# Kernel tuning notes

Measured on AMD Instinct MI355X. Metric: run time of the kernel, lower is better.

## Reference

```python
import jax, jax.numpy as jnp
import numpy as np

B, N, D = 8, 1024, 768
R, SH = 10, 2
H = R + SH            # 12 total heads
DH = D // H           # 64
DF = 2 * D            # FFN hidden


def _layernorm(x, g, b, eps=1e-5):
    mu = jnp.mean(x, axis=-1, keepdims=True)
    var = jnp.var(x, axis=-1, keepdims=True)
    return (x - mu) * jax.lax.rsqrt(var + eps) * g + b


def setup_inputs() -> dict:
    key = jax.random.key(0)
    ks = jax.random.split(key, 12)
    s = 0.02
    inp = {
        'nodes': jax.random.normal(ks[0], (B, N, D), dtype=jnp.float32),
        'relation_mask': jax.random.uniform(ks[1], (B, N, N, R), dtype=jnp.float32),
        'node_mask': jax.random.randint(ks[2], (B, N), 0, 2).astype(bool),
        'Wq': jax.random.normal(ks[3], (D, D), dtype=jnp.float32) * s,
        'bq': jnp.zeros((D,), jnp.float32),
        'Wk': jax.random.normal(ks[4], (D, D), dtype=jnp.float32) * s,
        'bk': jnp.zeros((D,), jnp.float32),
        'Wv': jax.random.normal(ks[5], (D, D), dtype=jnp.float32) * s,
        'bv': jnp.zeros((D,), jnp.float32),
        'Wo': jax.random.normal(ks[6], (D, D), dtype=jnp.float32) * s,
        'bo': jnp.zeros((D,), jnp.float32),
        'ln1_g': jnp.ones((D,), jnp.float32),
        'ln1_b': jnp.zeros((D,), jnp.float32),
        'W1': jax.random.normal(ks[7], (DF, D), dtype=jnp.float32) * s,
        'b1': jnp.zeros((DF,), jnp.float32),
        'W2': jax.random.normal(ks[8], (D, DF), dtype=jnp.float32) * s,
        'b2': jnp.zeros((D,), jnp.float32),
        'ln2_g': jnp.ones((D,), jnp.float32),
        'ln2_b': jnp.zeros((D,), jnp.float32),
    }
    return inp


def reference(nodes, relation_mask, node_mask, Wq, bq, Wk, bk, Wv, bv, Wo, bo,
              ln1_g, ln1_b, W1, b1, W2, b2, ln2_g, ln2_b):
    neg_inf = jnp.float32(-jnp.inf)
    # projections -> [B, H, N, DH]
    q = (nodes @ Wq.T + bq).reshape(B, N, H, DH).transpose(0, 2, 1, 3)
    k = (nodes @ Wk.T + bk).reshape(B, N, H, DH).transpose(0, 2, 1, 3)
    v = (nodes @ Wv.T + bv).reshape(B, N, H, DH).transpose(0, 2, 1, 3)
    scores = jnp.einsum('bhqd,bhkd->bhqk', q, k) / jnp.sqrt(jnp.float32(DH))
    # relation-typed gating on first R heads
    rel_gate = relation_mask.transpose(0, 3, 1, 2)          # [B, R, N, N]
    typed = jnp.where(rel_gate < 1e-4, neg_inf, scores[:, :R])
    scores = jnp.concatenate([typed, scores[:, R:]], axis=1)
    # key padding mask
    key_mask = node_mask[:, None, None, :]                  # [B,1,1,N]
    scores = jnp.where(key_mask, scores, neg_inf)
    attn = jax.nn.softmax(scores, axis=-1)
    attn = jnp.nan_to_num(attn, nan=0.0)                    # rows with no valid keys -> 0
    out = jnp.einsum('bhqk,bhkd->bhqd', attn, v)
    out = out.transpose(0, 2, 1, 3).reshape(B, N, D)
    out = out @ Wo.T + bo
    h = _layernorm(nodes + out, ln1_g, ln1_b)
    ffn = jax.nn.gelu(h @ W1.T + b1, approximate=False) @ W2.T + b2
    h = _layernorm(h + ffn, ln2_g, ln2_b)
    return h
```

## Files before the change

### kernel.cpp

```cpp
#include <hip/hip_runtime.h>
#include <stdint.h>
#include <math.h>

typedef unsigned short u16;
typedef __bf16 bf16x8 __attribute__((ext_vector_type(8)));
typedef __bf16 bf16x2 __attribute__((ext_vector_type(2)));
typedef unsigned short u16x8 __attribute__((ext_vector_type(8)));
typedef float f32x4 __attribute__((ext_vector_type(4)));

#define DEVI __device__ __forceinline__

constexpr int B_ = 8, N_ = 1024, D_ = 768, H_ = 12, DH_ = 64, DF_ = 1536;

DEVI u16 f2bu(float f) {
  unsigned x = __builtin_bit_cast(unsigned, f);
  x += 0x7FFFu + ((x >> 16) & 1u);
  return (u16)(x >> 16);
}
DEVI float b2f(u16 u) { return __builtin_bit_cast(float, (unsigned)u << 16); }

DEVI bf16x8 ld_frag(const u16* p) {
  return __builtin_bit_cast(bf16x8, *(const u16x8*)p);
}

DEVI void gload_lds16(const u16* g, u16* l) {
  __builtin_amdgcn_global_load_lds(
      (const __attribute__((address_space(1))) void*)g,
      (__attribute__((address_space(3))) void*)l, 16, 0, 0);
}

struct CvtArgs {
  const float* src[7];
  u16* dst[7];
  int n4[7];
  int start[8];
};
__global__ __launch_bounds__(256)
void prep_all(CvtArgs a, const float* __restrict__ rel, const int* __restrict__ nm,
              u16* __restrict__ mp) {
  const int gb0 = blockIdx.x;
  const int t = threadIdx.x;
  if (gb0 < 2048) {
    const int b = gb0 >> 8, q0 = ((gb0 >> 2) & 63) * 16, k0 = (gb0 & 3) * 256;
    __shared__ u16 w12[16][256];
    const int key_ok = nm[(b << 10) + k0 + t];
    const float th = 1e-4f;
#pragma unroll 1
    for (int it = 0; it < 16; ++it) {
      unsigned bits;
      if (!key_ok) {
        bits = 0xFFFu;
      } else {
        const size_t idx = (((size_t)(b << 10) + q0 + it) << 10) + k0 + t;
        const float2* rp = (const float2*)(rel + idx * 10);
        float2 a0 = rp[0], a1 = rp[1], a2 = rp[2], a3 = rp[3], a4 = rp[4];
        bits  = (a0.x < th ? 1u : 0u)   | (a0.y < th ? 2u : 0u)
              | (a1.x < th ? 4u : 0u)   | (a1.y < th ? 8u : 0u)
              | (a2.x < th ? 16u : 0u)  | (a2.y < th ? 32u : 0u)
              | (a3.x < th ? 64u : 0u)  | (a3.y < th ? 128u : 0u)
              | (a4.x < th ? 256u : 0u) | (a4.y < th ? 512u : 0u);
      }
      w12[it][t ^ ((it & 7) << 1)] = (u16)bits;
    }
    __syncthreads();
    const int ql = t & 15, kt = t >> 4;
    unsigned wv[16];
#pragma unroll
    for (int j2 = 0; j2 < 8; ++j2) {
      const int e = (kt * 16 + j2 * 2) ^ ((ql & 7) << 1);
      wv[j2 * 2] = w12[ql][e];
      wv[j2 * 2 + 1] = w12[ql][e + 1];
    }
#pragma unroll
    for (int h = 0; h < 12; ++h) {
      unsigned word = 0;
#pragma unroll
      for (int j = 0; j < 16; ++j) word |= ((wv[j] >> h) & 1u) << j;
      mp[(((size_t)(b * H_ + h)) * (N_ / 16) + (k0 >> 4) + kt) * N_ + q0 + ql] = (u16)word;
    }
  } else {
    int j = 0;
    while (gb0 >= a.start[j + 1]) ++j;
    const int i = (gb0 - a.start[j]) * 256 + t;
    if (i >= a.n4[j]) return;
    float4 v = ((const float4*)a.src[j])[i];
    ushort4 o;
    o.x = f2bu(v.x); o.y = f2bu(v.y); o.z = f2bu(v.z); o.w = f2bu(v.w);
    ((ushort4*)a.dst[j])[i] = o;
  }
}

template<int EPI>
DEVI void gemm_body(const u16* __restrict__ A, const u16* __restrict__ Bm,
                    const float* __restrict__ bias0, const float* __restrict__ bias1,
                    const float* __restrict__ residf, const u16* __restrict__ residb,
                    u16* __restrict__ out0, u16* __restrict__ out1,
                    int N, int K, int bx, int by,
                    u16 (&As)[3][128 * 32], u16 (&Bs)[3][128 * 32]) {
  const int t = threadIdx.x;
  const int w = t >> 6, l = t & 63;
  const int li = l & 15, grp = l >> 4;
  const int n0 = bx * 128, m0 = by * 128;
  const int wr = w >> 1, wc = w & 1;

  f32x4 acc[4][4] = {};

  const int arow = w * 16 + (l >> 2);
  const int acol = (l & 3) * 8;
  const u16* Ag = A + (size_t)(m0 + arow) * K + acol;
  const u16* Bg = Bm + (size_t)(n0 + arow) * K + acol;
  const int NT = K >> 5;

  auto stage = [&](int buf, int kt) {
    u16* Asw = &As[buf][(w * 16) * 32];
    u16* Bsw = &Bs[buf][(w * 16) * 32];
    const int k0 = kt * 32;
    gload_lds16(Ag + k0, Asw);
    gload_lds16(Ag + (size_t)64 * K + k0, Asw + 64 * 32);
    gload_lds16(Bg + k0, Bsw);
    gload_lds16(Bg + (size_t)64 * K + k0, Bsw + 64 * 32);
  };

  stage(0, 0); stage(1, 1);
  asm volatile("s_waitcnt vmcnt(4)\n\ts_barrier" ::: "memory");

  for (int kt = 0; kt < NT; ++kt) {
    const int bt = kt % 3;
    const bool pre = (kt + 2 < NT);
    if (pre) stage((kt + 2) % 3, kt + 2);
    bf16x8 af[4], bfr[4];
#pragma unroll
    for (int m = 0; m < 4; ++m)
      af[m] = ld_frag(&As[bt][(wr * 64 + m * 16 + li) * 32 + grp * 8]);
#pragma unroll
    for (int n = 0; n < 4; ++n)
      bfr[n] = ld_frag(&Bs[bt][(wc * 64 + n * 16 + li) * 32 + grp * 8]);
    __builtin_amdgcn_s_setprio(1);
#pragma unroll
    for (int m = 0; m < 4; ++m)
#pragma unroll
      for (int n = 0; n < 4; ++n)
        acc[m][n] = __builtin_amdgcn_mfma_f32_16x16x32_bf16(af[m], bfr[n], acc[m][n], 0, 0, 0);
    __builtin_amdgcn_s_setprio(0);
    if (pre) asm volatile("s_waitcnt vmcnt(4) lgkmcnt(0)\n\ts_barrier" ::: "memory");
    else     asm volatile("s_waitcnt vmcnt(0) lgkmcnt(0)\n\ts_barrier" ::: "memory");
  }

#pragma unroll
  for (int m = 0; m < 4; ++m) {
#pragma unroll
    for (int n = 0; n < 4; ++n) {
#pragma unroll
      for (int j = 0; j < 4; ++j) {
        const int row = m0 + wr * 64 + m * 16 + grp * 4 + j;
        const int col = n0 + wc * 64 + n * 16 + li;
        float v = acc[m][n][j];
        if constexpr (EPI == 0) {
          v += (col < D_) ? bias0[col] : bias1[col - D_];
          if (col < D_) v *= 0.125f;
          const int b = row >> 10, i = row & (N_ - 1);
          int c2 = (col < D_) ? col : col - D_;
          u16* dst = (col < D_) ? out0 : out1;
          dst[(((size_t)(b * H_ + (c2 >> 6))) * N_ + i) * DH_ + (c2 & 63)] = f2bu(v);
        } else if constexpr (EPI == 1) {
          v += bias0[row];
          const int b = col >> 10, i = col & (N_ - 1);
          out0[(((size_t)(b * H_ + (row >> 6))) * DH_ + (row & 63)) * N_ + i] = f2bu(v);
        } else if constexpr (EPI == 2) {
          v += bias0[col] + residf[(size_t)row * N + col];
          out0[(size_t)row * N + col] = f2bu(v);
        } else if constexpr (EPI == 3) {
          v += bias0[col];
          float gel = 0.5f * v * (1.0f + erff(v * 0.70710678118654752440f));
          out0[(size_t)row * N + col] = f2bu(gel);
        } else {
          v += bias0[col] + b2f(residb[(size_t)row * N + col]);
          out0[(size_t)row * N + col] = f2bu(v);
        }
      }
    }
  }
}

template<int EPI>
__global__ __launch_bounds__(256, 3)
void gemm_bt(const u16* __restrict__ A, const u16* __restrict__ Bm,
             const float* __restrict__ bias0,
             const float* __restrict__ residf, const u16* __restrict__ residb,
             u16* __restrict__ out0, int N, int K) {
  __shared__ u16 As[3][128 * 32];
  __shared__ u16 Bs[3][128 * 32];
  const int nwg = gridDim.x * gridDim.y;
  int id = blockIdx.y * gridDim.x + blockIdx.x;
  id = (id & 7) * (nwg >> 3) + (id >> 3);
  const int by = id / gridDim.x;
  const int bx = id - by * gridDim.x;
  gemm_body<EPI>(A, Bm, bias0, nullptr, residf, residb, out0, nullptr,
                 N, K, bx, by, As, Bs);
}

__global__ __launch_bounds__(256, 3)
void gemm_qkv(const u16* __restrict__ Xbf, const u16* __restrict__ Wqk,
              const u16* __restrict__ Wv,
              const float* __restrict__ bq, const float* __restrict__ bk,
              const float* __restrict__ bv,
              u16* __restrict__ qb, u16* __restrict__ kb, u16* __restrict__ vTb) {
  __shared__ u16 As[3][128 * 32];
  __shared__ u16 Bs[3][128 * 32];
  constexpr int nwg = 1152;
  int id = blockIdx.x;
  id = (id & 7) * (nwg >> 3) + (id >> 3);
  if (id < 768) {
    const int by = id / 12, bx = id - by * 12;
    gemm_body<0>(Xbf, Wqk, bq, bk, nullptr, nullptr, qb, kb,
                 1536, 768, bx, by, As, Bs);
  } else {
    const int v = id - 768;
    const int by = v / 64, bx = v - by * 64;
    gemm_body<1>(Wv, Xbf, bv, nullptr, nullptr, nullptr, vTb, nullptr,
                 8192, 768, bx, by, As, Bs);
  }
}

__global__ __launch_bounds__(512, 4)
void attn(const u16* __restrict__ q, const u16* __restrict__ k, const u16* __restrict__ vT,
          const u16* __restrict__ mp, u16* __restrict__ outp) {
  const int nwg = gridDim.x;
  const int p = blockIdx.x;
  const int lid = (p & 7) * (nwg >> 3) + (p >> 3);
  const int bh_i = lid >> 3;
  const int qblk = lid & 7;
  const int b = bh_i / H_, h = bh_i - (bh_i / H_) * H_;
  const int w = threadIdx.x >> 6, l = threadIdx.x & 63;
  const int li = l & 15, grp = l >> 4;
  const int qw = qblk * 128 + w * 16;
  const size_t bh = (size_t)bh_i;

  __shared__ u16 Kt[2][64 * 64];
  __shared__ u16 Vt[2][64 * 64];
  __shared__ u16 P[8][16 * 64];

  const u16* kbase = k + bh * N_ * DH_;
  const u16* vbase = vT + bh * DH_ * N_;

  const int srow_off = l >> 3;
  const int sg = l & 7;
  const int r0 = w * 8;
  auto stageK = [&](int buf, int kj0) {
    const int row = r0 + srow_off;
    const int gp = sg ^ (row & 7);
    gload_lds16(kbase + (size_t)(kj0 + row) * DH_ + gp * 8, &Kt[buf][r0 * 64]);
  };
  auto stageV = [&](int buf, int kj0) {
    const int row = r0 + srow_off;
    const int gp = sg ^ (row & 7);
    gload_lds16(vbase + (size_t)row * N_ + kj0 + gp * 8, &Vt[buf][r0 * 64]);
  };

  const u16* qp = q + (bh * N_ + qw) * DH_;
  const bf16x8 bq0 = ld_frag(qp + li * DH_ + grp * 8);
  const bf16x8 bq1 = ld_frag(qp + li * DH_ + 32 + grp * 8);

  f32x4 accO[4] = {};
  float m = -INFINITY, lsum = 0.f;

  u16* Pw = &P[w][0];
  const int sw = (li & 7) << 3;
  const int prow = li * 64;
  const u16* mrow = mp + bh * (N_ / 16) * N_ + qw + li;

  stageK(0, 0); stageV(0, 0);
  __syncthreads();
  int cur = 0;

  for (int kj0 = 0; kj0 < N_; kj0 += 64) {
    if (kj0 + 64 < N_) { stageK(cur ^ 1, kj0 + 64); stageV(cur ^ 1, kj0 + 64); }
    unsigned mword[4];
#pragma unroll
    for (int t = 0; t < 4; ++t) mword[t] = mrow[(size_t)((kj0 >> 4) + t) * N_];

    f32x4 s[4];
    __builtin_amdgcn_s_setprio(1);
#pragma unroll
    for (int t = 0; t < 4; ++t) {
      const int row = t * 16 + li;
      const int rs = row & 7;
      const bf16x8 ka0 = ld_frag(&Kt[cur][row * 64 + ((grp ^ rs) * 8)]);
      const bf16x8 ka1 = ld_frag(&Kt[cur][row * 64 + (((grp + 4) ^ rs) * 8)]);
      f32x4 z = {0.f, 0.f, 0.f, 0.f};
      z = __builtin_amdgcn_mfma_f32_16x16x32_bf16(ka0, bq0, z, 0, 0, 0);
      z = __builtin_amdgcn_mfma_f32_16x16x32_bf16(ka1, bq1, z, 0, 0, 0);
      s[t] = z;
    }
    __builtin_amdgcn_s_setprio(0);

    float sv[16];
#pragma unroll
    for (int t = 0; t < 4; ++t) {
      const unsigned mb = (mword[t] >> (grp * 4)) & 0xFu;
#pragma unroll
      for (int j = 0; j < 4; ++j)
        sv[t * 4 + j] = ((mb >> j) & 1u) ? -INFINITY : s[t][j];
    }
    const float a0 = fmaxf(fmaxf(sv[0], sv[1]), sv[2]);
    const float a1 = fmaxf(fmaxf(sv[3], sv[4]), sv[5]);
    const float a2 = fmaxf(fmaxf(sv[6], sv[7]), sv[8]);
    const float a3 = fmaxf(fmaxf(sv[9], sv[10]), sv[11]);
    const float a4 = fmaxf(fmaxf(sv[12], sv[13]), sv[14]);
    float rmax = fmaxf(fmaxf(fmaxf(a0, a1), fmaxf(a2, a3)), fmaxf(a4, sv[15]));
    rmax = fmaxf(rmax, __shfl_xor(rmax, 16));
    rmax = fmaxf(rmax, __shfl_xor(rmax, 32));
    if (!__all(rmax <= m + 8.f)) {
      const float mnew = fmaxf(m, rmax);
      const float scal = (m == -INFINITY) ? 0.f : __expf(m - mnew);
      lsum *= scal;
#pragma unroll
      for (int t2 = 0; t2 < 4; ++t2) accO[t2] *= scal;
      m = mnew;
    }
    const float msafe = (m == -INFINITY) ? 0.f : m;
    float psum = 0.f;
    float pv[16];
#pragma unroll
    for (int i = 0; i < 16; ++i) {
      const float e = __expf(sv[i] - msafe);
      pv[i] = e;
      psum += e;
    }
    psum += __shfl_xor(psum, 16);
    psum += __shfl_xor(psum, 32);
    lsum += psum;
#pragma unroll
    for (int t = 0; t < 4; ++t) {
      bf16x2 plo = { (__bf16)pv[t * 4 + 0], (__bf16)pv[t * 4 + 1] };
      bf16x2 phi = { (__bf16)pv[t * 4 + 2], (__bf16)pv[t * 4 + 3] };
      uint2 pk;
      pk.x = __builtin_bit_cast(unsigned, plo);
      pk.y = __builtin_bit_cast(unsigned, phi);
      *(uint2*)&Pw[prow + ((t * 16 + grp * 4) ^ sw)] = pk;
    }
    __builtin_amdgcn_s_setprio(1);
#pragma unroll
    for (int kc = 0; kc < 2; ++kc) {
      const bf16x8 pb = ld_frag(&Pw[prow + ((kc * 32 + grp * 8) ^ sw)]);
#pragma unroll
      for (int t2 = 0; t2 < 4; ++t2) {
        const int row = t2 * 16 + li;
        const bf16x8 va = ld_frag(&Vt[cur][row * 64 + (((kc * 4 + grp) ^ (row & 7)) * 8)]);
        accO[t2] = __builtin_amdgcn_mfma_f32_16x16x32_bf16(va, pb, accO[t2], 0, 0, 0);
      }
    }
    __builtin_amdgcn_s_setprio(0);
    __syncthreads();
    cur ^= 1;
  }
  const float inv = (lsum > 0.f) ? 1.0f / lsum : 0.f;
  u16* op = outp + ((size_t)b * N_ + qw + li) * D_ + h * DH_;
#pragma unroll
  for (int t2 = 0; t2 < 4; ++t2) {
    bf16x2 o01 = { (__bf16)(accO[t2][0] * inv), (__bf16)(accO[t2][1] * inv) };
    bf16x2 o23 = { (__bf16)(accO[t2][2] * inv), (__bf16)(accO[t2][3] * inv) };
    uint2 ov;
    ov.x = __builtin_bit_cast(unsigned, o01);
    ov.y = __builtin_bit_cast(unsigned, o23);
    *(uint2*)&op[t2 * 16 + grp * 4] = ov;
  }
}

template<int OUTF32>
__global__ __launch_bounds__(256)
void ln_kernel(const u16* __restrict__ x, const float* __restrict__ g,
               const float* __restrict__ be, u16* __restrict__ ybf,
               float* __restrict__ yf) {
  const int row = blockIdx.x;
  const int t = threadIdx.x;
  const u16* xr = x + (size_t)row * D_;
  const float v0 = b2f(xr[t]), v1 = b2f(xr[t + 256]), v2 = b2f(xr[t + 512]);
  float s = v0 + v1 + v2;
  float s2 = v0 * v0 + v1 * v1 + v2 * v2;
#pragma unroll
  for (int d = 1; d < 64; d <<= 1) { s += __shfl_xor(s, d); s2 += __shfl_xor(s2, d); }
  __shared__ float red[8];
  const int w = t >> 6;
  if ((t & 63) == 0) { red[w] = s; red[4 + w] = s2; }
  __syncthreads();
  s = red[0] + red[1] + red[2] + red[3];
  s2 = red[4] + red[5] + red[6] + red[7];
  const float mu = s * (1.0f / D_);
  const float var = fmaxf(s2 * (1.0f / D_) - mu * mu, 0.0f);
  const float rstd = rsqrtf(var + 1e-5f);
#pragma unroll
  for (int c = 0; c < 3; ++c) {
    const int idx = t + c * 256;
    const float vv = (c == 0) ? v0 : (c == 1) ? v1 : v2;
    const float o = (vv - mu) * rstd * g[idx] + be[idx];
    if constexpr (OUTF32) yf[(size_t)row * D_ + idx] = o;
    else ybf[(size_t)row * D_ + idx] = f2bu(o);
  }
}

extern "C" void kernel_launch(void* const* d_in, const int* in_sizes, int n_in,
                              void* d_out, int out_size, void* d_ws, size_t ws_size,
                              hipStream_t stream) {
  (void)in_sizes; (void)n_in; (void)out_size; (void)ws_size;
  const float* nodes = (const float*)d_in[0];
  const float* rel   = (const float*)d_in[1];
  const int*   nmask = (const int*)d_in[2];
  const float* Wq = (const float*)d_in[3];
  const float* bq = (const float*)d_in[4];
  const float* Wk = (const float*)d_in[5];
  const float* bk = (const float*)d_in[6];
  const float* Wv = (const float*)d_in[7];
  const float* bv = (const float*)d_in[8];
  const float* Wo = (const float*)d_in[9];
  const float* bo = (const float*)d_in[10];
  const float* ln1g = (const float*)d_in[11];
  const float* ln1b = (const float*)d_in[12];
  const float* W1 = (const float*)d_in[13];
  const float* b1 = (const float*)d_in[14];
  const float* W2 = (const float*)d_in[15];
  const float* b2 = (const float*)d_in[16];
  const float* ln2g = (const float*)d_in[17];
  const float* ln2b = (const float*)d_in[18];
  float* out = (float*)d_out;

  char* ws = (char*)d_ws;
  u16* Wqk_bf = (u16*)(ws + 0);
  u16* Wv_bf  = (u16*)(ws + 2359296);
  u16* Wo_bf  = (u16*)(ws + 3538944);
  u16* W1_bf  = (u16*)(ws + 4718592);
  u16* W2_bf  = (u16*)(ws + 7077888);
  u16* Xbf    = (u16*)(ws + 9437184);
  u16* qb     = (u16*)(ws + 22020096);
  u16* kb     = (u16*)(ws + 34603008);
  u16* vTb    = (u16*)(ws + 47185920);
  u16* mwb    = (u16*)(ws + 59768832);
  u16* prehb  = (u16*)(ws + 22020096);
  u16* hbf    = (u16*)(ws + 47185920);
  u16* f1b    = (u16*)(ws + 59768832);
  u16* preob  = (u16*)(ws + 84934656);
  u16* attno  = Xbf;

  const dim3 blk(256);
  CvtArgs ca;
  ca.src[0] = Wq; ca.src[1] = Wk; ca.src[2] = Wv; ca.src[3] = Wo;
  ca.src[4] = W1; ca.src[5] = W2; ca.src[6] = nodes;
  ca.dst[0] = Wqk_bf; ca.dst[1] = Wqk_bf + 768 * 768; ca.dst[2] = Wv_bf;
  ca.dst[3] = Wo_bf; ca.dst[4] = W1_bf; ca.dst[5] = W2_bf; ca.dst[6] = Xbf;
  ca.n4[0] = ca.n4[1] = ca.n4[2] = ca.n4[3] = 147456;
  ca.n4[4] = ca.n4[5] = 294912; ca.n4[6] = 1572864;
  ca.start[0] = 2048; ca.start[1] = 2624; ca.start[2] = 3200; ca.start[3] = 3776;
  ca.start[4] = 4352; ca.start[5] = 5504; ca.start[6] = 6656; ca.start[7] = 12800;
  prep_all<<<12800, blk, 0, stream>>>(ca, rel, nmask, mwb);
  gemm_qkv<<<1152, blk, 0, stream>>>(Xbf, Wqk_bf, Wv_bf, bq, bk, bv, qb, kb, vTb);
  attn<<<768, dim3(512), 0, stream>>>(qb, kb, vTb, mwb, attno);
  gemm_bt<2><<<dim3(6, 64), blk, 0, stream>>>(attno, Wo_bf, bo, nodes, nullptr,
                                              prehb, 768, 768);
  ln_kernel<0><<<8192, blk, 0, stream>>>(prehb, ln1g, ln1b, hbf, nullptr);
  gemm_bt<3><<<dim3(12, 64), blk, 0, stream>>>(hbf, W1_bf, b1, nullptr, nullptr,
                                               f1b, 1536, 768);
  gemm_bt<4><<<dim3(6, 64), blk, 0, stream>>>(f1b, W2_bf, b2, nullptr, hbf,
                                              preob, 768, 1536);
  ln_kernel<1><<<8192, blk, 0, stream>>>(preob, ln2g, ln2b, nullptr, out);
}
```

Baseline: 298.5 us.

## Use exp2 softmax, warp-per-row layernorm, and bf16 residual for Wo GEMM

Three separate changes. The Q scale now folds in log2(e), so attention can use exp2f instead of __expf, with the rescale threshold adjusted to match. LayerNorm now handles one row per wavefront with vectorized loads and stores, removing the shared-memory reduction and __syncthreads. The output projection reads its residual from the bf16 copy of nodes instead of fp32, so attention output moves to its own workspace buffer; this adds rounding error on the residual path.

```diff
diff --git a/kernel.cpp b/kernel.cpp
--- a/kernel.cpp
+++ b/kernel.cpp
@@ -6,11 +6,14 @@
 typedef __bf16 bf16x8 __attribute__((ext_vector_type(8)));
 typedef __bf16 bf16x2 __attribute__((ext_vector_type(2)));
 typedef unsigned short u16x8 __attribute__((ext_vector_type(8)));
+typedef unsigned short u16x4 __attribute__((ext_vector_type(4)));
 typedef float f32x4 __attribute__((ext_vector_type(4)));
 
 #define DEVI __device__ __forceinline__
 
 constexpr int B_ = 8, N_ = 1024, D_ = 768, H_ = 12, DH_ = 64, DF_ = 1536;
+constexpr float QSCALE = 0.18033688011112042f;
+constexpr float THR2 = 11.5415603f;
 
 DEVI u16 f2bu(float f) {
   unsigned x = __builtin_bit_cast(unsigned, f);
@@ -93,7 +96,7 @@
 template<int EPI>
 DEVI void gemm_body(const u16* __restrict__ A, const u16* __restrict__ Bm,
                     const float* __restrict__ bias0, const float* __restrict__ bias1,
-                    const float* __restrict__ residf, const u16* __restrict__ residb,
+                    const u16* __restrict__ residb,
                     u16* __restrict__ out0, u16* __restrict__ out1,
                     int N, int K, int bx, int by,
                     u16 (&As)[3][128 * 32], u16 (&Bs)[3][128 * 32]) {
@@ -157,7 +160,7 @@
         float v = acc[m][n][j];
         if constexpr (EPI == 0) {
           v += (col < D_) ? bias0[col] : bias1[col - D_];
-          if (col < D_) v *= 0.125f;
+          if (col < D_) v *= QSCALE;
           const int b = row >> 10, i = row & (N_ - 1);
           int c2 = (col < D_) ? col : col - D_;
           u16* dst = (col < D_) ? out0 : out1;
@@ -166,9 +169,6 @@
           v += bias0[row];
           const int b = col >> 10, i = col & (N_ - 1);
           out0[(((size_t)(b * H_ + (row >> 6))) * DH_ + (row & 63)) * N_ + i] = f2bu(v);
-        } else if constexpr (EPI == 2) {
-          v += bias0[col] + residf[(size_t)row * N + col];
-          out0[(size_t)row * N + col] = f2bu(v);
         } else if constexpr (EPI == 3) {
           v += bias0[col];
           float gel = 0.5f * v * (1.0f + erff(v * 0.70710678118654752440f));
@@ -185,8 +185,7 @@
 template<int EPI>
 __global__ __launch_bounds__(256, 3)
 void gemm_bt(const u16* __restrict__ A, const u16* __restrict__ Bm,
-             const float* __restrict__ bias0,
-             const float* __restrict__ residf, const u16* __restrict__ residb,
+             const float* __restrict__ bias0, const u16* __restrict__ residb,
              u16* __restrict__ out0, int N, int K) {
   __shared__ u16 As[3][128 * 32];
   __shared__ u16 Bs[3][128 * 32];
@@ -195,7 +194,7 @@
   id = (id & 7) * (nwg >> 3) + (id >> 3);
   const int by = id / gridDim.x;
   const int bx = id - by * gridDim.x;
-  gemm_body<EPI>(A, Bm, bias0, nullptr, residf, residb, out0, nullptr,
+  gemm_body<EPI>(A, Bm, bias0, nullptr, residb, out0, nullptr,
                  N, K, bx, by, As, Bs);
 }
 
@@ -212,12 +211,12 @@
   id = (id & 7) * (nwg >> 3) + (id >> 3);
   if (id < 768) {
     const int by = id / 12, bx = id - by * 12;
-    gemm_body<0>(Xbf, Wqk, bq, bk, nullptr, nullptr, qb, kb,
+    gemm_body<0>(Xbf, Wqk, bq, bk, nullptr, qb, kb,
                  1536, 768, bx, by, As, Bs);
   } else {
     const int v = id - 768;
     const int by = v / 64, bx = v - by * 64;
-    gemm_body<1>(Wv, Xbf, bv, nullptr, nullptr, nullptr, vTb, nullptr,
+    gemm_body<1>(Wv, Xbf, bv, nullptr, nullptr, vTb, nullptr,
                  8192, 768, bx, by, As, Bs);
   }
 }
@@ -310,9 +309,9 @@
     float rmax = fmaxf(fmaxf(fmaxf(a0, a1), fmaxf(a2, a3)), fmaxf(a4, sv[15]));
     rmax = fmaxf(rmax, __shfl_xor(rmax, 16));
     rmax = fmaxf(rmax, __shfl_xor(rmax, 32));
-    if (!__all(rmax <= m + 8.f)) {
+    if (!__all(rmax <= m + THR2)) {
       const float mnew = fmaxf(m, rmax);
-      const float scal = (m == -INFINITY) ? 0.f : __expf(m - mnew);
+      const float scal = (m == -INFINITY) ? 0.f : exp2f(m - mnew);
       lsum *= scal;
 #pragma unroll
       for (int t2 = 0; t2 < 4; ++t2) accO[t2] *= scal;
@@ -323,7 +322,7 @@
     float pv[16];
 #pragma unroll
     for (int i = 0; i < 16; ++i) {
-      const float e = __expf(sv[i] - msafe);
+      const float e = exp2f(sv[i] - msafe);
       pv[i] = e;
       psum += e;
     }
@@ -372,30 +371,53 @@
 void ln_kernel(const u16* __restrict__ x, const float* __restrict__ g,
                const float* __restrict__ be, u16* __restrict__ ybf,
                float* __restrict__ yf) {
-  const int row = blockIdx.x;
-  const int t = threadIdx.x;
-  const u16* xr = x + (size_t)row * D_;
-  const float v0 = b2f(xr[t]), v1 = b2f(xr[t + 256]), v2 = b2f(xr[t + 512]);
-  float s = v0 + v1 + v2;
-  float s2 = v0 * v0 + v1 * v1 + v2 * v2;
+  const int w = threadIdx.x >> 6, lane = threadIdx.x & 63;
+  const int row = blockIdx.x * 4 + w;
+  const u16* xr = x + (size_t)row * D_ + lane * 12;
+  u16x4 p0 = *(const u16x4*)(xr);
+  u16x4 p1 = *(const u16x4*)(xr + 4);
+  u16x4 p2 = *(const u16x4*)(xr + 8);
+  float v[12];
+#pragma unroll
+  for (int i = 0; i < 4; ++i) {
+    v[i] = b2f(p0[i]); v[4 + i] = b2f(p1[i]); v[8 + i] = b2f(p2[i]);
+  }
+  float s = 0.f, s2 = 0.f;
+#pragma unroll
+  for (int i = 0; i < 12; ++i) { s += v[i]; s2 += v[i] * v[i]; }
 #pragma unroll
   for (int d = 1; d < 64; d <<= 1) { s += __shfl_xor(s, d); s2 += __shfl_xor(s2, d); }
-  __shared__ float red[8];
-  const int w = t >> 6;
-  if ((t & 63) == 0) { red[w] = s; red[4 + w] = s2; }
-  __syncthreads();
-  s = red[0] + red[1] + red[2] + red[3];
-  s2 = red[4] + red[5] + red[6] + red[7];
   const float mu = s * (1.0f / D_);
   const float var = fmaxf(s2 * (1.0f / D_) - mu * mu, 0.0f);
   const float rstd = rsqrtf(var + 1e-5f);
+  const float* gp = g + lane * 12;
+  const float* bp = be + lane * 12;
+  float o[12];
 #pragma unroll
   for (int c = 0; c < 3; ++c) {
-    const int idx = t + c * 256;
-    const float vv = (c == 0) ? v0 : (c == 1) ? v1 : v2;
-    const float o = (vv - mu) * rstd * g[idx] + be[idx];
-    if constexpr (OUTF32) yf[(size_t)row * D_ + idx] = o;
-    else ybf[(size_t)row * D_ + idx] = f2bu(o);
+    float4 gv = *(const float4*)(gp + c * 4);
+    float4 bv = *(const float4*)(bp + c * 4);
+    o[c * 4 + 0] = (v[c * 4 + 0] - mu) * rstd * gv.x + bv.x;
+    o[c * 4 + 1] = (v[c * 4 + 1] - mu) * rstd * gv.y + bv.y;
+    o[c * 4 + 2] = (v[c * 4 + 2] - mu) * rstd * gv.z + bv.z;
+    o[c * 4 + 3] = (v[c * 4 + 3] - mu) * rstd * gv.w + bv.w;
+  }
+  if constexpr (OUTF32) {
+    float* yr = yf + (size_t)row * D_ + lane * 12;
+#pragma unroll
+    for (int c = 0; c < 3; ++c) {
+      float4 ov = { o[c * 4], o[c * 4 + 1], o[c * 4 + 2], o[c * 4 + 3] };
+      *(float4*)(yr + c * 4) = ov;
+    }
+  } else {
+    u16* yr = ybf + (size_t)row * D_ + lane * 12;
+#pragma unroll
+    for (int c = 0; c < 3; ++c) {
+      u16x4 ov;
+      ov[0] = f2bu(o[c * 4 + 0]); ov[1] = f2bu(o[c * 4 + 1]);
+      ov[2] = f2bu(o[c * 4 + 2]); ov[3] = f2bu(o[c * 4 + 3]);
+      *(u16x4*)(yr + c * 4) = ov;
+    }
   }
 }
 
@@ -439,7 +461,7 @@
   u16* hbf    = (u16*)(ws + 47185920);
   u16* f1b    = (u16*)(ws + 59768832);
   u16* preob  = (u16*)(ws + 84934656);
-  u16* attno  = Xbf;
+  u16* attno  = (u16*)(ws + 100663296);
 
   const dim3 blk(256);
   CvtArgs ca;
@@ -454,12 +476,12 @@
   prep_all<<<12800, blk, 0, stream>>>(ca, rel, nmask, mwb);
   gemm_qkv<<<1152, blk, 0, stream>>>(Xbf, Wqk_bf, Wv_bf, bq, bk, bv, qb, kb, vTb);
   attn<<<768, dim3(512), 0, stream>>>(qb, kb, vTb, mwb, attno);
-  gemm_bt<2><<<dim3(6, 64), blk, 0, stream>>>(attno, Wo_bf, bo, nodes, nullptr,
+  gemm_bt<4><<<dim3(6, 64), blk, 0, stream>>>(attno, Wo_bf, bo, Xbf,
                                               prehb, 768, 768);
-  ln_kernel<0><<<8192, blk, 0, stream>>>(prehb, ln1g, ln1b, hbf, nullptr);
-  gemm_bt<3><<<dim3(12, 64), blk, 0, stream>>>(hbf, W1_bf, b1, nullptr, nullptr,
+  ln_kernel<0><<<2048, blk, 0, stream>>>(prehb, ln1g, ln1b, hbf, nullptr);
+  gemm_bt<3><<<dim3(12, 64), blk, 0, stream>>>(hbf, W1_bf, b1, nullptr,
                                                f1b, 1536, 768);
-  gemm_bt<4><<<dim3(6, 64), blk, 0, stream>>>(f1b, W2_bf, b2, nullptr, hbf,
+  gemm_bt<4><<<dim3(6, 64), blk, 0, stream>>>(f1b, W2_bf, b2, hbf,
                                               preob, 768, 1536);
-  ln_kernel<1><<<8192, blk, 0, stream>>>(preob, ln2g, ln2b, nullptr, out);
-}
+  ln_kernel<1><<<2048, blk, 0, stream>>>(preob, ln2g, ln2b, nullptr, out);
+}
```

Measured after the change: 303.2 us. About the same (+1.6%).
